# Optimization experiments

Measured on AMD Instinct MI355X. Metric: run time of the kernel, lower is better.

## Reference

```python
import jax, jax.numpy as jnp
import numpy as np

B, C, H, W = 8, 96, 160, 320
MH, MW = 4, 4

def setup_inputs() -> dict:
    key = jax.random.key(0)
    k1, k2 = jax.random.split(key)
    feat1 = jax.random.normal(k1, (B, C, H, W), dtype=jnp.float32)
    feat2 = jax.random.normal(k2, (B, C, H, W), dtype=jnp.float32)
    return {"feat1": feat1, "feat2": feat2, "max_offset_h": MH, "max_offset_w": MW}

def reference(feat1, feat2, max_offset_h, max_offset_w):
    # feat1, feat2: [B, C, H, W]
    # cost[b, d, h, w] = sum_c feat1[b,c,h,w] * feat2[b,c,h+dh,w+dw]
    # with (dh, dw) enumerating the (2*mh+1)*(2*mw+1) offset window and
    # zero padding outside image boundaries.
    b, c, h, w = feat1.shape
    mh, mw = max_offset_h, max_offset_w
    padded = jnp.pad(feat2, ((0, 0), (0, 0), (mh, mh), (mw, mw)))
    costs = []
    for dh in range(2 * mh + 1):
        for dw in range(2 * mw + 1):
            shifted = jax.lax.dynamic_slice(padded, (0, 0, dh, dw), (b, c, h, w))
            costs.append(jnp.sum(feat1 * shifted, axis=1))  # [B, H, W]
    return jnp.stack(costs, axis=1)  # [B, (2mh+1)*(2mw+1), H, W]
```

## Files before the change

kernel.cpp:

```cpp
#include <hip/hip_runtime.h>

#define B_   8
#define C_   96
#define H_   160
#define W_   320
#define ND   9
#define NDD  81
#define TH   16
#define TW   16
#define KC   8
#define NCH  12
#define F1PLANE 256
#define F2PLANE 576
#define F2OFF   (KC*F1PLANE)
#define BUFW    (KC*(F1PLANE+F2PLANE))
#define LDSWORDS (2*BUFW)

#define AS1 __attribute__((address_space(1)))
#define AS3 __attribute__((address_space(3)))

__device__ __forceinline__ void gld16(const float* gp, const float* lp) {
    __builtin_amdgcn_global_load_lds((const AS1 float*)gp,
                                     (AS3 float*)(unsigned long long)lp, 16, 0, 0);
}
__device__ __forceinline__ void gld4(const float* gp, const float* lp) {
    __builtin_amdgcn_global_load_lds((const AS1 float*)gp,
                                     (AS3 float*)(unsigned long long)lp, 4, 0, 0);
}

__global__ __launch_bounds__(576)
void corr_kernel(const float* __restrict__ f1g,
                 const float* __restrict__ f2g,
                 float* __restrict__ out)
{
    __shared__ float lds[LDSWORDS];

    const int tid  = threadIdx.x;
    const int wave = tid >> 6;
    const int lane = tid & 63;
    const int row  = lane >> 2;
    const int colb = (lane & 3) * 4;

    const int bid  = blockIdx.x;
    const int ebid = (bid & 7) * 200 + (bid >> 3);
    const int b    = ebid / 200;
    const int rr   = ebid - b * 200;
    const int by   = rr / 20;
    const int bx   = rr - by * 20;
    const int x0 = bx * TW, y0 = by * TH;
    const int HWi  = H_ * W_;
    const int base1 = b * C_ * HWi;

    for (int i = tid; i < LDSWORDS; i += 576) lds[i] = 0.f;

    const int f1goff = base1 + (y0 + (lane >> 2)) * W_ + x0 + (lane & 3) * 4;
    int f2g0, f2g1, f2g2; bool f2p0, f2p1, f2p2;
    {
        int fl, r, c, y, x;
        fl = lane * 4;       r = fl / 24; c = fl - r * 24; y = y0 - 4 + r; x = x0 - 4 + c;
        f2p0 = (y >= 0) & (y < H_) & (x >= 0) & (x + 4 <= W_);  f2g0 = base1 + y * W_ + x;
        fl = 256 + lane * 4; r = fl / 24; c = fl - r * 24; y = y0 - 4 + r; x = x0 - 4 + c;
        f2p1 = (y >= 0) & (y < H_) & (x >= 0) & (x + 4 <= W_);  f2g1 = base1 + y * W_ + x;
        fl = 512 + lane;     r = fl / 24; c = fl - r * 24; y = y0 - 4 + r; x = x0 - 4 + c;
        f2p2 = (y >= 0) & (y < H_) & (x >= 0) & (x < W_);       f2g2 = base1 + y * W_ + x;
    }

    const int f1readbase = row * 16 + colb;
    const int f2readbase = (row + wave) * 24 + colb;

    auto stage = [&](int cb, int wbase) {
        for (int s = wave; s < 4 * KC; s += 9) {
            const int ch   = s >> 2;
            const int part = s & 3;
            const int coff = (cb + ch) * HWi;
            if (part == 0) {
                gld16(f1g + f1goff + coff, &lds[wbase + ch * F1PLANE]);
            } else if (part == 1) {
                if (f2p0) gld16(f2g + f2g0 + coff, &lds[wbase + F2OFF + ch * F2PLANE]);
            } else if (part == 2) {
                if (f2p1) gld16(f2g + f2g1 + coff, &lds[wbase + F2OFF + ch * F2PLANE + 256]);
            } else {
                if (f2p2) gld4(f2g + f2g2 + coff, &lds[wbase + F2OFF + ch * F2PLANE + 512]);
            }
        }
    };

    float4 acc0, acc1, acc2, acc3, acc4, acc5, acc6, acc7, acc8;
    acc0 = acc1 = acc2 = acc3 = acc4 = acc5 = acc6 = acc7 = acc8 = make_float4(0.f, 0.f, 0.f, 0.f);

#define STEPD(A, P, e0, e1, e2, e3)                             \
        A.x = fmaf(P.x, e0, A.x);                               \
        A.y = fmaf(P.y, e1, A.y);                               \
        A.z = fmaf(P.z, e2, A.z);                               \
        A.w = fmaf(P.w, e3, A.w);

#define COMPC(c) {                                                                  \
        const float4 P  = *(const float4*)&lds[rb_ + c * F1PLANE + f1readbase];     \
        const float4 q0 = *(const float4*)&lds[rb_ + F2OFF + c * F2PLANE + f2readbase];     \
        const float4 q1 = *(const float4*)&lds[rb_ + F2OFF + c * F2PLANE + f2readbase + 4]; \
        const float4 q2 = *(const float4*)&lds[rb_ + F2OFF + c * F2PLANE + f2readbase + 8]; \
        STEPD(acc0, P, q0.x, q0.y, q0.z, q0.w)                                      \
        STEPD(acc1, P, q0.y, q0.z, q0.w, q1.x)                                      \
        STEPD(acc2, P, q0.z, q0.w, q1.x, q1.y)                                      \
        STEPD(acc3, P, q0.w, q1.x, q1.y, q1.z)                                      \
        STEPD(acc4, P, q1.x, q1.y, q1.z, q1.w)                                      \
        STEPD(acc5, P, q1.y, q1.z, q1.w, q2.x)                                      \
        STEPD(acc6, P, q1.z, q1.w, q2.x, q2.y)                                      \
        STEPD(acc7, P, q1.w, q2.x, q2.y, q2.z)                                      \
        STEPD(acc8, P, q2.x, q2.y, q2.z, q2.w)                                      \
    }
#define REP8(M) M(0) M(1) M(2) M(3) M(4) M(5) M(6) M(7)

    __syncthreads();
    stage(0, 0);
    __syncthreads();

#pragma unroll 1
    for (int ch = 0; ch < NCH; ++ch) {
        const int rb_ = (ch & 1) * BUFW;
        if (ch + 1 < NCH) stage((ch + 1) * KC, BUFW - rb_);
        REP8(COMPC)
        __syncthreads();
    }

    const int gy = y0 + row;
    const int gx = x0 + colb;
#define STORED(d) {                                                                   \
        float* op_ = out + (size_t)((b * NDD + wave * ND + d) * H_ + gy) * W_ + gx;   \
        *(float4*)op_ = acc##d; }
    STORED(0) STORED(1) STORED(2) STORED(3) STORED(4)
    STORED(5) STORED(6) STORED(7) STORED(8)
}

extern "C" void kernel_launch(void* const* d_in, const int* in_sizes, int n_in,
                              void* d_out, int out_size, void* d_ws, size_t ws_size,
                              hipStream_t stream)
{
    const float* f1 = (const float*)d_in[0];
    const float* f2 = (const float*)d_in[1];
    float* out = (float*)d_out;
    corr_kernel<<<dim3(1600), 576, 0, stream>>>(f1, f2, out);
}
```

Measured before the change: 245.0 us.

## Triple-buffer LDS staging with vmcnt waits and zero-source loads for padding

Moves from a double buffer to a triple buffer in LDS and prefetches two chunks ahead. Each wave now waits for its own loads with explicit s_waitcnt vmcnt counts and then a raw s_barrier, so the second __syncthreads per iteration is gone. Out-of-bounds feat2 loads now read from a global zero array, which removes the upfront LDS zero fill and the predicated skips. Load work is also reassigned so eight waves each load one channel and the ninth wave loads the tail column. The risks are more LDS per block, which may lower occupancy, and hand-counted vmcnt values that must exactly match the number of loads issued per wave.

```diff
diff --git a/kernel.cpp b/kernel.cpp
--- a/kernel.cpp
+++ b/kernel.cpp
@@ -14,10 +14,13 @@
 #define F2PLANE 576
 #define F2OFF   (KC*F1PLANE)
 #define BUFW    (KC*(F1PLANE+F2PLANE))
-#define LDSWORDS (2*BUFW)
+#define NBUF    3
+#define LDSWORDS (NBUF*BUFW)
 
 #define AS1 __attribute__((address_space(1)))
 #define AS3 __attribute__((address_space(3)))
+
+__device__ float g_zero[512];
 
 __device__ __forceinline__ void gld16(const float* gp, const float* lp) {
     __builtin_amdgcn_global_load_lds((const AS1 float*)gp,
@@ -51,36 +54,43 @@
     const int HWi  = H_ * W_;
     const int base1 = b * C_ * HWi;
 
-    for (int i = tid; i < LDSWORDS; i += 576) lds[i] = 0.f;
+    const float* f1src = f1g + base1 + (y0 + row) * W_ + x0 + colb;
 
-    const int f1goff = base1 + (y0 + (lane >> 2)) * W_ + x0 + (lane & 3) * 4;
-    int f2g0, f2g1, f2g2; bool f2p0, f2p1, f2p2;
+    const float* p0; const float* p1; bool inb0, inb1;
     {
         int fl, r, c, y, x;
         fl = lane * 4;       r = fl / 24; c = fl - r * 24; y = y0 - 4 + r; x = x0 - 4 + c;
-        f2p0 = (y >= 0) & (y < H_) & (x >= 0) & (x + 4 <= W_);  f2g0 = base1 + y * W_ + x;
+        inb0 = (y >= 0) & (y < H_) & (x >= 0) & (x + 4 <= W_);
+        p0 = f2g + base1 + y * W_ + x;
         fl = 256 + lane * 4; r = fl / 24; c = fl - r * 24; y = y0 - 4 + r; x = x0 - 4 + c;
-        f2p1 = (y >= 0) & (y < H_) & (x >= 0) & (x + 4 <= W_);  f2g1 = base1 + y * W_ + x;
-        fl = 512 + lane;     r = fl / 24; c = fl - r * 24; y = y0 - 4 + r; x = x0 - 4 + c;
-        f2p2 = (y >= 0) & (y < H_) & (x >= 0) & (x < W_);       f2g2 = base1 + y * W_ + x;
+        inb1 = (y >= 0) & (y < H_) & (x >= 0) & (x + 4 <= W_);
+        p1 = f2g + base1 + y * W_ + x;
     }
+    const float* pT; bool inbT;
+    {
+        int fl = 512 + lane;
+        int r = fl / 24, c = fl - r * 24;
+        int y = y0 - 4 + r, x = x0 - 4 + c;
+        inbT = (y >= 0) & (y < H_) & (x >= 0) & (x < W_);
+        pT = f2g + base1 + y * W_ + x;
+    }
+    const float* zl = g_zero + lane * 4;
+    const float* zt = g_zero + lane;
 
     const int f1readbase = row * 16 + colb;
     const int f2readbase = (row + wave) * 24 + colb;
 
-    auto stage = [&](int cb, int wbase) {
-        for (int s = wave; s < 4 * KC; s += 9) {
-            const int ch   = s >> 2;
-            const int part = s & 3;
-            const int coff = (cb + ch) * HWi;
-            if (part == 0) {
-                gld16(f1g + f1goff + coff, &lds[wbase + ch * F1PLANE]);
-            } else if (part == 1) {
-                if (f2p0) gld16(f2g + f2g0 + coff, &lds[wbase + F2OFF + ch * F2PLANE]);
-            } else if (part == 2) {
-                if (f2p1) gld16(f2g + f2g1 + coff, &lds[wbase + F2OFF + ch * F2PLANE + 256]);
-            } else {
-                if (f2p2) gld4(f2g + f2g2 + coff, &lds[wbase + F2OFF + ch * F2PLANE + 512]);
+    auto stage = [&](int cb, int bufb) {
+        if (wave < 8) {
+            const int coff = (cb + wave) * HWi;
+            gld16(f1src + coff, &lds[bufb + wave * F1PLANE]);
+            gld16(inb0 ? p0 + coff : zl, &lds[bufb + F2OFF + wave * F2PLANE]);
+            gld16(inb1 ? p1 + coff : zl, &lds[bufb + F2OFF + wave * F2PLANE + 256]);
+        } else {
+#pragma unroll
+            for (int c = 0; c < 8; ++c) {
+                gld4(inbT ? pT + (cb + c) * HWi : zt,
+                     &lds[bufb + F2OFF + c * F2PLANE + 512]);
             }
         }
     };
@@ -111,16 +121,21 @@
     }
 #define REP8(M) M(0) M(1) M(2) M(3) M(4) M(5) M(6) M(7)
 
-    __syncthreads();
     stage(0, 0);
-    __syncthreads();
+    stage(KC, BUFW);
 
 #pragma unroll 1
-    for (int ch = 0; ch < NCH; ++ch) {
-        const int rb_ = (ch & 1) * BUFW;
-        if (ch + 1 < NCH) stage((ch + 1) * KC, BUFW - rb_);
+    for (int k = 0; k < NCH; ++k) {
+        if (k + 1 < NCH) {
+            if (wave < 8) { asm volatile("s_waitcnt vmcnt(3)" ::: "memory"); }
+            else          { asm volatile("s_waitcnt vmcnt(8)" ::: "memory"); }
+        } else {
+            asm volatile("s_waitcnt vmcnt(0)" ::: "memory");
+        }
+        __builtin_amdgcn_s_barrier();
+        if (k + 2 < NCH) stage((k + 2) * KC, ((k + 2) % 3) * BUFW);
+        const int rb_ = (k % 3) * BUFW;
         REP8(COMPC)
-        __syncthreads();
     }
 
     const int gy = y0 + row;
```

New measurement: 229.6 us. -6.3%, faster.

## Swizzle feat2 LDS tile rows and simplify per-wave async staging

Applied to the files above, without the earlier changes.

Each feat2 channel plane in LDS becomes 24 rows of 32 floats, up from a packed 24×24. The 4-float column chunks are XOR-swizzled by row so the shifted float4 reads spread across LDS banks. Staging now uses eight waves, one channel each, issuing only 16-byte global-to-LDS loads, which removes the 4-byte tail loads and the part-dispatch branching. The channel loop is unrolled by two so buffer offsets are compile-time constants. The cost is a larger LDS footprint and an idle ninth wave during staging.

```diff
diff --git a/kernel.cpp b/kernel.cpp
--- a/kernel.cpp
+++ b/kernel.cpp
@@ -11,7 +11,7 @@
 #define KC   8
 #define NCH  12
 #define F1PLANE 256
-#define F2PLANE 576
+#define F2PLANE 768
 #define F2OFF   (KC*F1PLANE)
 #define BUFW    (KC*(F1PLANE+F2PLANE))
 #define LDSWORDS (2*BUFW)
@@ -23,12 +23,8 @@
     __builtin_amdgcn_global_load_lds((const AS1 float*)gp,
                                      (AS3 float*)(unsigned long long)lp, 16, 0, 0);
 }
-__device__ __forceinline__ void gld4(const float* gp, const float* lp) {
-    __builtin_amdgcn_global_load_lds((const AS1 float*)gp,
-                                     (AS3 float*)(unsigned long long)lp, 4, 0, 0);
-}
 
-__global__ __launch_bounds__(576)
+__global__ __launch_bounds__(576, 8)
 void corr_kernel(const float* __restrict__ f1g,
                  const float* __restrict__ f2g,
                  float* __restrict__ out)
@@ -39,7 +35,8 @@
     const int wave = tid >> 6;
     const int lane = tid & 63;
     const int row  = lane >> 2;
-    const int colb = (lane & 3) * 4;
+    const int m    = lane & 3;
+    const int colb = m << 2;
 
     const int bid  = blockIdx.x;
     const int ebid = (bid & 7) * 200 + (bid >> 3);
@@ -49,39 +46,38 @@
     const int bx   = rr - by * 20;
     const int x0 = bx * TW, y0 = by * TH;
     const int HWi  = H_ * W_;
-    const int base1 = b * C_ * HWi;
 
-    for (int i = tid; i < LDSWORDS; i += 576) lds[i] = 0.f;
+    const float* f1b = f1g + (size_t)b * C_ * HWi;
+    const float* f2b = f2g + (size_t)b * C_ * HWi;
 
-    const int f1goff = base1 + (y0 + (lane >> 2)) * W_ + x0 + (lane & 3) * 4;
-    int f2g0, f2g1, f2g2; bool f2p0, f2p1, f2p2;
-    {
-        int fl, r, c, y, x;
-        fl = lane * 4;       r = fl / 24; c = fl - r * 24; y = y0 - 4 + r; x = x0 - 4 + c;
-        f2p0 = (y >= 0) & (y < H_) & (x >= 0) & (x + 4 <= W_);  f2g0 = base1 + y * W_ + x;
-        fl = 256 + lane * 4; r = fl / 24; c = fl - r * 24; y = y0 - 4 + r; x = x0 - 4 + c;
-        f2p1 = (y >= 0) & (y < H_) & (x >= 0) & (x + 4 <= W_);  f2g1 = base1 + y * W_ + x;
-        fl = 512 + lane;     r = fl / 24; c = fl - r * 24; y = y0 - 4 + r; x = x0 - 4 + c;
-        f2p2 = (y >= 0) & (y < H_) & (x >= 0) & (x < W_);       f2g2 = base1 + y * W_ + x;
-    }
+    const int f1so = (y0 + row) * W_ + x0 + colb;
+    const int  rr8 = lane >> 3;
+    const int  cbl = (lane & 7) ^ rr8;
+    const int  fx  = x0 - 4 + (cbl << 2);
+    const bool xok = (cbl <= 5) & (fx >= 0) & (fx <= W_ - 4);
+    const int  gy0 = y0 - 4 + rr8;
+    const bool ok0 = xok & (gy0 >= 0);
+    const bool ok1 = xok;
+    const bool ok1b = ok1 & (gy0 + 8 < H_);
+    const bool ok2 = xok & (gy0 + 16 < H_);
+    const int  off0 = gy0 * W_ + fx;
 
-    const int f1readbase = row * 16 + colb;
-    const int f2readbase = (row + wave) * 24 + colb;
+    const int rW = row + wave;
+    const int sw = rW & 7;
+    const int o0 = rW * 32 + (((m + 0) ^ sw) << 2);
+    const int o1 = rW * 32 + (((m + 1) ^ sw) << 2);
+    const int o2 = rW * 32 + (((m + 2) ^ sw) << 2);
+    const int f1ro = lane << 2;
 
-    auto stage = [&](int cb, int wbase) {
-        for (int s = wave; s < 4 * KC; s += 9) {
-            const int ch   = s >> 2;
-            const int part = s & 3;
-            const int coff = (cb + ch) * HWi;
-            if (part == 0) {
-                gld16(f1g + f1goff + coff, &lds[wbase + ch * F1PLANE]);
-            } else if (part == 1) {
-                if (f2p0) gld16(f2g + f2g0 + coff, &lds[wbase + F2OFF + ch * F2PLANE]);
-            } else if (part == 2) {
-                if (f2p1) gld16(f2g + f2g1 + coff, &lds[wbase + F2OFF + ch * F2PLANE + 256]);
-            } else {
-                if (f2p2) gld4(f2g + f2g2 + coff, &lds[wbase + F2OFF + ch * F2PLANE + 512]);
-            }
+    auto stage = [&](int cb, int bufb) {
+        if (wave < 8) {
+            const int co = (cb + wave) * HWi;
+            gld16(f1b + co + f1so, &lds[bufb + wave * F1PLANE]);
+            const float* p = f2b + co + off0;
+            const float* l = &lds[bufb + F2OFF + wave * F2PLANE];
+            if (ok0)  gld16(p,             l);
+            if (ok1b) gld16(p + 8  * W_,   l + 256);
+            if (ok2)  gld16(p + 16 * W_,   l + 512);
         }
     };
 
@@ -94,11 +90,11 @@
         A.z = fmaf(P.z, e2, A.z);                               \
         A.w = fmaf(P.w, e3, A.w);
 
-#define COMPC(c) {                                                                  \
-        const float4 P  = *(const float4*)&lds[rb_ + c * F1PLANE + f1readbase];     \
-        const float4 q0 = *(const float4*)&lds[rb_ + F2OFF + c * F2PLANE + f2readbase];     \
-        const float4 q1 = *(const float4*)&lds[rb_ + F2OFF + c * F2PLANE + f2readbase + 4]; \
-        const float4 q2 = *(const float4*)&lds[rb_ + F2OFF + c * F2PLANE + f2readbase + 8]; \
+#define COMPC(c, RB) {                                                              \
+        const float4 P  = *(const float4*)&lds[(RB) + c * F1PLANE + f1ro];          \
+        const float4 q0 = *(const float4*)&lds[(RB) + F2OFF + c * F2PLANE + o0];    \
+        const float4 q1 = *(const float4*)&lds[(RB) + F2OFF + c * F2PLANE + o1];    \
+        const float4 q2 = *(const float4*)&lds[(RB) + F2OFF + c * F2PLANE + o2];    \
         STEPD(acc0, P, q0.x, q0.y, q0.z, q0.w)                                      \
         STEPD(acc1, P, q0.y, q0.z, q0.w, q1.x)                                      \
         STEPD(acc2, P, q0.z, q0.w, q1.x, q1.y)                                      \
@@ -109,18 +105,21 @@
         STEPD(acc7, P, q1.w, q2.x, q2.y, q2.z)                                      \
         STEPD(acc8, P, q2.x, q2.y, q2.z, q2.w)                                      \
     }
-#define REP8(M) M(0) M(1) M(2) M(3) M(4) M(5) M(6) M(7)
+#define CHUNK(RB) COMPC(0,RB) COMPC(1,RB) COMPC(2,RB) COMPC(3,RB) \
+                  COMPC(4,RB) COMPC(5,RB) COMPC(6,RB) COMPC(7,RB)
 
+    for (int t = tid; t < LDSWORDS; t += 576) lds[t] = 0.f;
     __syncthreads();
     stage(0, 0);
-    __syncthreads();
 
 #pragma unroll 1
-    for (int ch = 0; ch < NCH; ++ch) {
-        const int rb_ = (ch & 1) * BUFW;
-        if (ch + 1 < NCH) stage((ch + 1) * KC, BUFW - rb_);
-        REP8(COMPC)
+    for (int kk = 0; kk < NCH / 2; ++kk) {
         __syncthreads();
+        stage((2 * kk + 1) * KC, BUFW);
+        CHUNK(0)
+        __syncthreads();
+        if (kk < NCH / 2 - 1) stage((2 * kk + 2) * KC, 0);
+        CHUNK(BUFW)
     }
 
     const int gy = y0 + row;
```

Measured after the change: 317.5 us. 1.3x slower.
